# Kernel optimization log

Measured on AMD Instinct MI355X. Metric: run time of the kernel, lower is better.

The kernel has to match this reference:

```python
import jax, jax.numpy as jnp
import numpy as np

N = 100000        # nodes
E = 1600000       # edges (avg degree 16)
F_IN = 64         # num_node_features
NHID = 64         # args.nhid
NCLS = 16         # num_classes
K1 = 8            # Chebyshev order of conv1


def setup_inputs() -> dict:
    key = jax.random.key(0)
    k0, k1, k2, k3 = jax.random.split(key, 4)
    x = jax.random.normal(k0, (N, F_IN), dtype=jnp.float32)
    edge_index = jax.random.randint(k1, (2, E), 0, N, dtype=jnp.int32)
    # ChebConv params: K linear maps (no per-lin bias) + one shared bias
    W1 = jax.random.normal(k2, (K1, F_IN, NHID), dtype=jnp.float32) * (1.0 / np.sqrt(F_IN))
    b1 = jnp.zeros((NHID,), dtype=jnp.float32)
    W2 = jax.random.normal(k3, (1, NHID, NCLS), dtype=jnp.float32) * (1.0 / np.sqrt(NHID))
    b2 = jnp.zeros((NCLS,), dtype=jnp.float32)
    return {"x": x, "edge_index": edge_index, "W1": W1, "b1": b1, "W2": W2, "b2": b2}


def _cheb_norm(edge_index, num_nodes):
    # PyG ChebConv.__norm__ with normalization='sym', lambda_max=2.0, unit edge weights:
    # remove self loops; L_hat = 2L/lambda_max - I = -D^{-1/2} A D^{-1/2}, diag = 0.
    row, col = edge_index[0], edge_index[1]
    nonself = (row != col).astype(jnp.float32)
    deg = jax.ops.segment_sum(nonself, row, num_segments=num_nodes)
    dinv = jnp.where(deg > 0, jax.lax.rsqrt(jnp.maximum(deg, 1.0)), 0.0)
    norm = -dinv[row] * dinv[col] * nonself
    return row, col, norm


def reference(x, edge_index, W1, b1, W2, b2):
    row, col, norm = _cheb_norm(edge_index, N)

    def prop(h):  # L_hat @ h via gather + scatter-add, [N,F]
        return jax.ops.segment_sum(h[col] * norm[:, None], row, num_segments=N)

    # conv1: ChebConv K=8 recursion  Tx_k = 2*L_hat*Tx_{k-1} - Tx_{k-2}
    tx_prev = x
    out = x @ W1[0]
    tx = prop(x)
    out = out + tx @ W1[1]
    for k in range(2, K1):
        tx_new = 2.0 * prop(tx) - tx_prev
        out = out + tx_new @ W1[k]
        tx_prev, tx = tx, tx_new
    h = jax.nn.relu(out + b1)
    # dropout: identity (eval mode)
    # conv2: ChebConv K=1 -> just Tx_0 = h
    logits = h @ W2[0] + b2
    return jax.nn.softmax(logits, axis=1)
```

## Files before the change

### kernel.cpp

```cpp
#include <hip/hip_runtime.h>
#include <hip/hip_fp16.h>

#define N_NODES 100000
#define N_EDGES 1600000
#define F 64
#define NCLS 16
#define K1 8
#define BSH 9
#define NBK 196
#define BROWS 512
#define BKCAP 9216
#define EPB 4096

using f16x8 = __attribute__((ext_vector_type(8))) _Float16;
using f32x4 = __attribute__((ext_vector_type(4))) float;

__global__ __launch_bounds__(256) void k_bucketA(const int* __restrict__ ei,
                                                 int* __restrict__ gcur,
                                                 int2* __restrict__ bk) {
    __shared__ int cnt[4][256];
    __shared__ int wbase[4][256];
    int tid = threadIdx.x;
    int w = tid >> 6;
    for (int i = tid; i < 1024; i += 256) ((int*)cnt)[i] = 0;
    __syncthreads();
    int rv[16], cv[16], packed[16];
    int e0 = blockIdx.x * EPB;
#pragma unroll
    for (int u = 0; u < 16; u++) {
        int e = e0 + u * 256 + tid;
        packed[u] = -1;
        if (e < N_EDGES) {
            rv[u] = ei[e];
            cv[u] = ei[N_EDGES + e];
            if (rv[u] != cv[u]) {
                int b = rv[u] >> BSH;
                int rank = atomicAdd(&cnt[w][b], 1);
                packed[u] = (rank << 8) | b;
            }
        }
    }
    __syncthreads();
    {
        int c0 = cnt[0][tid], c1 = cnt[1][tid], c2 = cnt[2][tid], c3 = cnt[3][tid];
        int tot = c0 + c1 + c2 + c3;
        int g = tot ? atomicAdd(&gcur[tid], tot) : 0;
        wbase[0][tid] = g;
        wbase[1][tid] = g + c0;
        wbase[2][tid] = g + c0 + c1;
        wbase[3][tid] = g + c0 + c1 + c2;
    }
    __syncthreads();
#pragma unroll
    for (int u = 0; u < 16; u++) {
        if (packed[u] >= 0) {
            int b = packed[u] & 255;
            int rank = packed[u] >> 8;
            bk[(size_t)b * BKCAP + wbase[w][b] + rank] = make_int2(rv[u], cv[u]);
        }
    }
}

__global__ __launch_bounds__(256) void k_degB(const int2* __restrict__ bk,
                                              const int* __restrict__ gcur,
                                              int* __restrict__ deg,
                                              float* __restrict__ dinv,
                                              int* __restrict__ rowptr) {
    __shared__ int hist[BROWS];
    __shared__ int sd[256];
    int b = blockIdx.x;
    int tid = threadIdx.x;
    for (int i = tid; i < BROWS; i += 256) hist[i] = 0;
    __syncthreads();
    int cnt = gcur[b];
    const int2* src = bk + (size_t)b * BKCAP;
    for (int i = tid; i < cnt; i += 256)
        atomicAdd(&hist[src[i].x & (BROWS - 1)], 1);
    __syncthreads();
    int v0 = hist[2 * tid], v1 = hist[2 * tid + 1];
    int s = v0 + v1;
    sd[tid] = s;
    __syncthreads();
    for (int d = 1; d < 256; d <<= 1) {
        int t = (tid >= d) ? sd[tid - d] : 0;
        __syncthreads();
        sd[tid] += t;
        __syncthreads();
    }
    int excl = sd[tid] - s;
    int rbase = b << BSH;
    int cbase = b * BKCAP;
    int gr0 = rbase + 2 * tid;
    int gr1 = gr0 + 1;
    if (gr0 < N_NODES) {
        deg[gr0] = v0;
        dinv[gr0] = v0 > 0 ? rsqrtf((float)v0) : 0.f;
        rowptr[gr0] = cbase + excl;
    }
    if (gr1 < N_NODES) {
        deg[gr1] = v1;
        dinv[gr1] = v1 > 0 ? rsqrtf((float)v1) : 0.f;
        rowptr[gr1] = cbase + excl + v0;
    }
}

__global__ __launch_bounds__(256) void k_fillB(const int2* __restrict__ bk,
                                               const int* __restrict__ gcur,
                                               const int* __restrict__ rowptr,
                                               const float* __restrict__ dinv,
                                               int2* __restrict__ csr_ew) {
    __shared__ int cur[BROWS];
    int b = blockIdx.x;
    for (int i = threadIdx.x; i < BROWS; i += 256) cur[i] = 0;
    __syncthreads();
    int cnt = gcur[b];
    const int2* src = bk + (size_t)b * BKCAP;
    for (int i = threadIdx.x; i < cnt; i += 256) {
        int2 rc = src[i];
        int rank = atomicAdd(&cur[rc.x & (BROWS - 1)], 1);
        float w = -dinv[rc.x] * dinv[rc.y];
        csr_ew[rowptr[rc.x] + rank] = make_int2(rc.y, __float_as_int(w));
    }
}

__global__ void k_cvt(const float* __restrict__ x, __half* __restrict__ t0) {
    int i = blockIdx.x * blockDim.x + threadIdx.x;
    int base = i * 4;
    if (base >= N_NODES * F) return;
    float4 v = *(const float4*)&x[base];
    __half2 a = __floats2half2_rn(v.x, v.y);
    __half2 b = __floats2half2_rn(v.z, v.w);
    *(__half2*)&t0[base] = a;
    *(__half2*)&t0[base + 2] = b;
}

__global__ void k_prepW(const float* __restrict__ W1, __half* __restrict__ Wf) {
    int t = blockIdx.x * blockDim.x + threadIdx.x;
    if (t >= K1 * 2 * 4 * 64) return;
    int lane = t & 63;
    int cb = (t >> 6) & 3;
    int fg = (t >> 8) & 1;
    int kidx = t >> 9;
    int col = cb * 16 + (lane & 15);
    int kbase = fg * 32 + (lane >> 4) * 8;
    f16x8 v;
#pragma unroll
    for (int j = 0; j < 8; j++)
        v[j] = (_Float16)W1[kidx * 4096 + (kbase + j) * 64 + col];
    *(f16x8*)(Wf + (size_t)t * 8) = v;
}

__global__ __launch_bounds__(256) void k_prop(const int* __restrict__ rowptr,
                                              const int* __restrict__ deg,
                                              const int2* __restrict__ csr_ew,
                                              const __half* __restrict__ src,
                                              const __half* __restrict__ prev,
                                              __half* __restrict__ dst,
                                              float alpha, float beta) {
    int wpair = (int)((blockIdx.x * blockDim.x + threadIdx.x) >> 6);
    int lane = threadIdx.x & 63;
    int nA = wpair * 2;
    if (nA >= N_NODES) return;
    int h = lane >> 5;
    int hl = lane & 31;
    int s3 = (lane >> 3) & 3;
    int fb = (lane & 7) * 8;
    int node = nA + h;
    bool valid = node < N_NODES;
    int cb  = valid ? rowptr[node] : 0;
    int end = valid ? cb + deg[node] : 0;

    float acc[8] = {};

    while (true) {
        int n_own = end - cb;
        if (n_own > 32) n_own = 32;
        if (n_own < 0) n_own = 0;
        int n_oth = __shfl(n_own, lane ^ 32, 64);
        int nmax = n_own > n_oth ? n_own : n_oth;
        if (nmax == 0) break;
        int2 e = make_int2(0, 0);
        if (hl < n_own) e = csr_ew[cb + hl];
        for (int j = 0; j < nmax; j += 16) {
            int cc[4];
            float ww[4];
#pragma unroll
            for (int g = 0; g < 4; g++) {
                int sl = (h << 5) | (j + g * 4 + s3);
                cc[g] = __shfl(e.x, sl, 64);
                ww[g] = __int_as_float(__shfl(e.y, sl, 64));
            }
            uint4 raw[4];
#pragma unroll
            for (int g = 0; g < 4; g++)
                raw[g] = *(const uint4*)(src + (size_t)cc[g] * F + fb);
#pragma unroll
            for (int g = 0; g < 4; g++) {
                float2 f0 = __half22float2(*(__half2*)&raw[g].x);
                float2 f1 = __half22float2(*(__half2*)&raw[g].y);
                float2 f2 = __half22float2(*(__half2*)&raw[g].z);
                float2 f3 = __half22float2(*(__half2*)&raw[g].w);
                acc[0] = fmaf(ww[g], f0.x, acc[0]);
                acc[1] = fmaf(ww[g], f0.y, acc[1]);
                acc[2] = fmaf(ww[g], f1.x, acc[2]);
                acc[3] = fmaf(ww[g], f1.y, acc[3]);
                acc[4] = fmaf(ww[g], f2.x, acc[4]);
                acc[5] = fmaf(ww[g], f2.y, acc[5]);
                acc[6] = fmaf(ww[g], f3.x, acc[6]);
                acc[7] = fmaf(ww[g], f3.y, acc[7]);
            }
        }
        cb += n_own;
    }

#pragma unroll
    for (int i = 0; i < 8; i++) {
        acc[i] += __shfl_xor(acc[i], 8, 64);
        acc[i] += __shfl_xor(acc[i], 16, 64);
    }

    if ((lane & 24) == 0 && valid) {
        float r[8];
#pragma unroll
        for (int i = 0; i < 8; i++) r[i] = alpha * acc[i];
        if (beta != 0.f) {
            uint4 pv = *(const uint4*)(prev + (size_t)node * F + fb);
            float2 p0 = __half22float2(*(__half2*)&pv.x);
            float2 p1 = __half22float2(*(__half2*)&pv.y);
            float2 p2 = __half22float2(*(__half2*)&pv.z);
            float2 p3 = __half22float2(*(__half2*)&pv.w);
            r[0] -= beta * p0.x; r[1] -= beta * p0.y;
            r[2] -= beta * p1.x; r[3] -= beta * p1.y;
            r[4] -= beta * p2.x; r[5] -= beta * p2.y;
            r[6] -= beta * p3.x; r[7] -= beta * p3.y;
        }
        uint4 outv;
        *(__half2*)&outv.x = __floats2half2_rn(r[0], r[1]);
        *(__half2*)&outv.y = __floats2half2_rn(r[2], r[3]);
        *(__half2*)&outv.z = __floats2half2_rn(r[4], r[5]);
        *(__half2*)&outv.w = __floats2half2_rn(r[6], r[7]);
        *(uint4*)(dst + (size_t)node * F + fb) = outv;
    }
}

__global__ __launch_bounds__(256) void k_fused_mfma(const __half* __restrict__ T,
                                                    const __half* __restrict__ Wf,
                                                    const float* __restrict__ b1,
                                                    const float* __restrict__ W2,
                                                    const float* __restrict__ b2,
                                                    float* __restrict__ y) {
    __shared__ float Ht[64][65];
    __shared__ float W2l[64 * 16];
    __shared__ float b2l[16];
    int tid = threadIdx.x;
    int lane = tid & 63;
    int w = tid >> 6;
    int ln15 = lane & 15;
    int lg = lane >> 4;
    int base = blockIdx.x * 64;

    for (int j = tid; j < 64 * 16; j += 256) W2l[j] = W2[j];
    if (tid < 16) b2l[tid] = b2[tid];

    int nd = base + (w << 4) + ln15;
    if (nd > N_NODES - 1) nd = N_NODES - 1;

    f32x4 acc0 = {0.f, 0.f, 0.f, 0.f};
    f32x4 acc1 = {0.f, 0.f, 0.f, 0.f};
    f32x4 acc2 = {0.f, 0.f, 0.f, 0.f};
    f32x4 acc3 = {0.f, 0.f, 0.f, 0.f};

    for (int s = 0; s < 16; s++) {
        int kidx = s >> 1;
        int fg = s & 1;
        f16x8 a = *(const f16x8*)(T + ((size_t)kidx * N_NODES + nd) * F + fg * 32 + lg * 8);
        const __half* wb = Wf + ((size_t)((kidx * 2 + fg) * 4) * 64 + lane) * 8;
        f16x8 b0 = *(const f16x8*)(wb);
        f16x8 b1f = *(const f16x8*)(wb + 64 * 8);
        f16x8 b2f = *(const f16x8*)(wb + 128 * 8);
        f16x8 b3f = *(const f16x8*)(wb + 192 * 8);
        acc0 = __builtin_amdgcn_mfma_f32_16x16x32_f16(a, b0, acc0, 0, 0, 0);
        acc1 = __builtin_amdgcn_mfma_f32_16x16x32_f16(a, b1f, acc1, 0, 0, 0);
        acc2 = __builtin_amdgcn_mfma_f32_16x16x32_f16(a, b2f, acc2, 0, 0, 0);
        acc3 = __builtin_amdgcn_mfma_f32_16x16x32_f16(a, b3f, acc3, 0, 0, 0);
    }

    int hrow = (w << 4) + (lg << 2);
    {
        float bb0 = b1[0 * 16 + ln15];
        float bb1 = b1[1 * 16 + ln15];
        float bb2 = b1[2 * 16 + ln15];
        float bb3 = b1[3 * 16 + ln15];
#pragma unroll
        for (int r = 0; r < 4; r++) {
            float h0 = acc0[r] + bb0;
            float h1 = acc1[r] + bb1;
            float h2 = acc2[r] + bb2;
            float h3 = acc3[r] + bb3;
            Ht[hrow + r][0 * 16 + ln15] = h0 > 0.f ? h0 : 0.f;
            Ht[hrow + r][1 * 16 + ln15] = h1 > 0.f ? h1 : 0.f;
            Ht[hrow + r][2 * 16 + ln15] = h2 > 0.f ? h2 : 0.f;
            Ht[hrow + r][3 * 16 + ln15] = h3 > 0.f ? h3 : 0.f;
        }
    }
    __syncthreads();

    int node = tid >> 2;
    int cg = tid & 3;
    int gnode = base + node;
    if (gnode >= N_NODES) return;
    float l0 = b2l[cg * 4 + 0], l1 = b2l[cg * 4 + 1], l2 = b2l[cg * 4 + 2], l3 = b2l[cg * 4 + 3];
    for (int f = 0; f < 64; f++) {
        float h = Ht[node][f];
        l0 = fmaf(h, W2l[f * 16 + cg * 4 + 0], l0);
        l1 = fmaf(h, W2l[f * 16 + cg * 4 + 1], l1);
        l2 = fmaf(h, W2l[f * 16 + cg * 4 + 2], l2);
        l3 = fmaf(h, W2l[f * 16 + cg * 4 + 3], l3);
    }
    float m = fmaxf(fmaxf(l0, l1), fmaxf(l2, l3));
    m = fmaxf(m, __shfl_xor(m, 1, 64));
    m = fmaxf(m, __shfl_xor(m, 2, 64));
    float e0 = expf(l0 - m), e1 = expf(l1 - m), e2 = expf(l2 - m), e3 = expf(l3 - m);
    float s = e0 + e1 + e2 + e3;
    s += __shfl_xor(s, 1, 64);
    s += __shfl_xor(s, 2, 64);
    float inv = 1.f / s;
    float4 o = make_float4(e0 * inv, e1 * inv, e2 * inv, e3 * inv);
    *(float4*)&y[(size_t)gnode * 16 + cg * 4] = o;
}


extern "C" void kernel_launch(void* const* d_in, const int* in_sizes, int n_in,
                              void* d_out, int out_size, void* d_ws, size_t ws_size,
                              hipStream_t stream) {
    const float* x  = (const float*)d_in[0];
    const int*   ei = (const int*)d_in[1];
    const float* W1 = (const float*)d_in[2];
    const float* b1 = (const float*)d_in[3];
    const float* W2 = (const float*)d_in[4];
    const float* b2 = (const float*)d_in[5];
    float* y = (float*)d_out;

    char* p = (char*)d_ws;
    auto alloc = [&](size_t bytes) {
        char* q = p;
        p += (bytes + 255) & ~(size_t)255;
        return q;
    };
    int*   deg    = (int*)alloc((size_t)N_NODES * 4);
    float* dinv   = (float*)alloc((size_t)N_NODES * 4);
    int*   rowptr = (int*)alloc((size_t)(N_NODES + 1) * 4);
    int*   gcur   = (int*)alloc(256 * 4);
    int2*  csr_ew = (int2*)alloc((size_t)NBK * BKCAP * 8);
    __half* T     = (__half*)alloc((size_t)K1 * N_NODES * F * 2);
    __half* Wf    = (__half*)alloc((size_t)K1 * 2 * 4 * 64 * 8 * 2);

    int2* bk = (int2*)T;

    hipMemsetAsync(gcur, 0, 256 * 4, stream);

    k_bucketA<<<(N_EDGES + EPB - 1) / EPB, 256, 0, stream>>>(ei, gcur, bk);
    k_degB<<<NBK, 256, 0, stream>>>(bk, gcur, deg, dinv, rowptr);
    k_fillB<<<NBK, 256, 0, stream>>>(bk, gcur, rowptr, dinv, csr_ew);
    k_prepW<<<16, 256, 0, stream>>>(W1, Wf);

    const size_t TSZ = (size_t)N_NODES * F;
    __half* Tk[K1];
    for (int k = 0; k < K1; k++) Tk[k] = T + (size_t)k * TSZ;

    k_cvt<<<(N_NODES * F / 4 + 255) / 256, 256, 0, stream>>>(x, Tk[0]);

    int npair = (N_NODES + 1) / 2;
    int prop_blocks = (npair + 3) / 4;
    k_prop<<<prop_blocks, 256, 0, stream>>>(rowptr, deg, csr_ew, Tk[0], Tk[0], Tk[1], 1.f, 0.f);
    for (int k = 2; k < K1; k++)
        k_prop<<<prop_blocks, 256, 0, stream>>>(rowptr, deg, csr_ew, Tk[k - 1], Tk[k - 2], Tk[k], 2.f, 1.f);

    int gemm_blocks = (N_NODES + 63) / 64;
    k_fused_mfma<<<gemm_blocks, 256, 0, stream>>>(T, Wf, b1, W2, b2, y);
}
```

Measured before the change: 324.6 us.

## Pack bucketed edges into 32 bits, fuse CSR fill into degree kernel, recompute edge weights

Bucketed edges are packed as a single 32-bit word holding the local row and the column, which halves bucket traffic. The degree/rowptr kernel now also does the per-bucket counting sort in shared memory and writes a column-only CSR, which removes the separate fill kernel. The propagation kernel stores only column indices and computes the weight as dinv[col] per edge, with -dinv[row] applied once per node. This halves CSR bytes read per edge but adds a dependent gather of dinv for each edge. The 36 KB shared-memory sort buffer may also lower occupancy of the CSR kernel.

```diff
diff --git a/kernel.cpp b/kernel.cpp
--- a/kernel.cpp
+++ b/kernel.cpp
@@ -11,30 +11,32 @@
 #define BROWS 512
 #define BKCAP 9216
 #define EPB 4096
+#define COLBITS 17
 
 using f16x8 = __attribute__((ext_vector_type(8))) _Float16;
 using f32x4 = __attribute__((ext_vector_type(4))) float;
 
 __global__ __launch_bounds__(256) void k_bucketA(const int* __restrict__ ei,
                                                  int* __restrict__ gcur,
-                                                 int2* __restrict__ bk) {
+                                                 unsigned* __restrict__ bk) {
     __shared__ int cnt[4][256];
     __shared__ int wbase[4][256];
     int tid = threadIdx.x;
     int w = tid >> 6;
     for (int i = tid; i < 1024; i += 256) ((int*)cnt)[i] = 0;
     __syncthreads();
-    int rv[16], cv[16], packed[16];
+    unsigned pe[16];
+    int packed[16];
     int e0 = blockIdx.x * EPB;
 #pragma unroll
     for (int u = 0; u < 16; u++) {
         int e = e0 + u * 256 + tid;
         packed[u] = -1;
         if (e < N_EDGES) {
-            rv[u] = ei[e];
-            cv[u] = ei[N_EDGES + e];
-            if (rv[u] != cv[u]) {
-                int b = rv[u] >> BSH;
+            int r = ei[e], c = ei[N_EDGES + e];
+            if (r != c) {
+                int b = r >> BSH;
+                pe[u] = ((unsigned)(r & (BROWS - 1)) << COLBITS) | (unsigned)c;
                 int rank = atomicAdd(&cnt[w][b], 1);
                 packed[u] = (rank << 8) | b;
             }
@@ -56,26 +58,29 @@
         if (packed[u] >= 0) {
             int b = packed[u] & 255;
             int rank = packed[u] >> 8;
-            bk[(size_t)b * BKCAP + wbase[w][b] + rank] = make_int2(rv[u], cv[u]);
-        }
-    }
-}
-
-__global__ __launch_bounds__(256) void k_degB(const int2* __restrict__ bk,
+            bk[(size_t)b * BKCAP + wbase[w][b] + rank] = pe[u];
+        }
+    }
+}
+
+__global__ __launch_bounds__(256) void k_csrB(const unsigned* __restrict__ bk,
                                               const int* __restrict__ gcur,
                                               int* __restrict__ deg,
                                               float* __restrict__ dinv,
-                                              int* __restrict__ rowptr) {
+                                              int* __restrict__ rowptr,
+                                              int* __restrict__ csr_col) {
     __shared__ int hist[BROWS];
+    __shared__ int cur[BROWS];
     __shared__ int sd[256];
+    __shared__ int sorted[BKCAP];
     int b = blockIdx.x;
     int tid = threadIdx.x;
-    for (int i = tid; i < BROWS; i += 256) hist[i] = 0;
+    for (int i = tid; i < BROWS; i += 256) { hist[i] = 0; cur[i] = 0; }
     __syncthreads();
     int cnt = gcur[b];
-    const int2* src = bk + (size_t)b * BKCAP;
+    const unsigned* src = bk + (size_t)b * BKCAP;
     for (int i = tid; i < cnt; i += 256)
-        atomicAdd(&hist[src[i].x & (BROWS - 1)], 1);
+        atomicAdd(&hist[src[i] >> COLBITS], 1);
     __syncthreads();
     int v0 = hist[2 * tid], v1 = hist[2 * tid + 1];
     int s = v0 + v1;
@@ -102,25 +107,19 @@
         dinv[gr1] = v1 > 0 ? rsqrtf((float)v1) : 0.f;
         rowptr[gr1] = cbase + excl + v0;
     }
-}
-
-__global__ __launch_bounds__(256) void k_fillB(const int2* __restrict__ bk,
-                                               const int* __restrict__ gcur,
-                                               const int* __restrict__ rowptr,
-                                               const float* __restrict__ dinv,
-                                               int2* __restrict__ csr_ew) {
-    __shared__ int cur[BROWS];
-    int b = blockIdx.x;
-    for (int i = threadIdx.x; i < BROWS; i += 256) cur[i] = 0;
-    __syncthreads();
-    int cnt = gcur[b];
-    const int2* src = bk + (size_t)b * BKCAP;
-    for (int i = threadIdx.x; i < cnt; i += 256) {
-        int2 rc = src[i];
-        int rank = atomicAdd(&cur[rc.x & (BROWS - 1)], 1);
-        float w = -dinv[rc.x] * dinv[rc.y];
-        csr_ew[rowptr[rc.x] + rank] = make_int2(rc.y, __float_as_int(w));
-    }
+    __syncthreads();
+    hist[2 * tid] = excl;
+    hist[2 * tid + 1] = excl + v0;
+    __syncthreads();
+    for (int i = tid; i < cnt; i += 256) {
+        unsigned e = src[i];
+        int rl = e >> COLBITS;
+        int pos = hist[rl] + atomicAdd(&cur[rl], 1);
+        sorted[pos] = (int)(e & ((1u << COLBITS) - 1));
+    }
+    __syncthreads();
+    for (int i = tid; i < cnt; i += 256)
+        csr_col[cbase + i] = sorted[i];
 }
 
 __global__ void k_cvt(const float* __restrict__ x, __half* __restrict__ t0) {
@@ -152,7 +151,8 @@
 
 __global__ __launch_bounds__(256) void k_prop(const int* __restrict__ rowptr,
                                               const int* __restrict__ deg,
-                                              const int2* __restrict__ csr_ew,
+                                              const int* __restrict__ csr_col,
+                                              const float* __restrict__ dinv,
                                               const __half* __restrict__ src,
                                               const __half* __restrict__ prev,
                                               __half* __restrict__ dst,
@@ -169,6 +169,7 @@
     bool valid = node < N_NODES;
     int cb  = valid ? rowptr[node] : 0;
     int end = valid ? cb + deg[node] : 0;
+    float dn = valid ? dinv[node] : 0.f;
 
     float acc[8] = {};
 
@@ -179,16 +180,20 @@
         int n_oth = __shfl(n_own, lane ^ 32, 64);
         int nmax = n_own > n_oth ? n_own : n_oth;
         if (nmax == 0) break;
-        int2 e = make_int2(0, 0);
-        if (hl < n_own) e = csr_ew[cb + hl];
+        int col = 0;
+        float dv = 0.f;
+        if (hl < n_own) {
+            col = csr_col[cb + hl];
+            dv = dinv[col];
+        }
         for (int j = 0; j < nmax; j += 16) {
             int cc[4];
             float ww[4];
 #pragma unroll
             for (int g = 0; g < 4; g++) {
                 int sl = (h << 5) | (j + g * 4 + s3);
-                cc[g] = __shfl(e.x, sl, 64);
-                ww[g] = __int_as_float(__shfl(e.y, sl, 64));
+                cc[g] = __shfl(col, sl, 64);
+                ww[g] = __shfl(dv, sl, 64);
             }
             uint4 raw[4];
 #pragma unroll
@@ -220,9 +225,10 @@
     }
 
     if ((lane & 24) == 0 && valid) {
+        float scale = -alpha * dn;
         float r[8];
 #pragma unroll
-        for (int i = 0; i < 8; i++) r[i] = alpha * acc[i];
+        for (int i = 0; i < 8; i++) r[i] = scale * acc[i];
         if (beta != 0.f) {
             uint4 pv = *(const uint4*)(prev + (size_t)node * F + fb);
             float2 p0 = __half22float2(*(__half2*)&pv.x);
@@ -347,21 +353,20 @@
         p += (bytes + 255) & ~(size_t)255;
         return q;
     };
-    int*   deg    = (int*)alloc((size_t)N_NODES * 4);
-    float* dinv   = (float*)alloc((size_t)N_NODES * 4);
-    int*   rowptr = (int*)alloc((size_t)(N_NODES + 1) * 4);
-    int*   gcur   = (int*)alloc(256 * 4);
-    int2*  csr_ew = (int2*)alloc((size_t)NBK * BKCAP * 8);
-    __half* T     = (__half*)alloc((size_t)K1 * N_NODES * F * 2);
-    __half* Wf    = (__half*)alloc((size_t)K1 * 2 * 4 * 64 * 8 * 2);
-
-    int2* bk = (int2*)T;
+    int*   deg     = (int*)alloc((size_t)N_NODES * 4);
+    float* dinv    = (float*)alloc((size_t)N_NODES * 4);
+    int*   rowptr  = (int*)alloc((size_t)N_NODES * 4);
+    int*   gcur    = (int*)alloc(256 * 4);
+    int*   csr_col = (int*)alloc((size_t)NBK * BKCAP * 4);
+    __half* T      = (__half*)alloc((size_t)K1 * N_NODES * F * 2);
+    __half* Wf     = (__half*)alloc((size_t)K1 * 2 * 4 * 64 * 8 * 2);
+
+    unsigned* bk = (unsigned*)T;
 
     hipMemsetAsync(gcur, 0, 256 * 4, stream);
 
     k_bucketA<<<(N_EDGES + EPB - 1) / EPB, 256, 0, stream>>>(ei, gcur, bk);
-    k_degB<<<NBK, 256, 0, stream>>>(bk, gcur, deg, dinv, rowptr);
-    k_fillB<<<NBK, 256, 0, stream>>>(bk, gcur, rowptr, dinv, csr_ew);
+    k_csrB<<<NBK, 256, 0, stream>>>(bk, gcur, deg, dinv, rowptr, csr_col);
     k_prepW<<<16, 256, 0, stream>>>(W1, Wf);
 
     const size_t TSZ = (size_t)N_NODES * F;
@@ -372,9 +377,9 @@
 
     int npair = (N_NODES + 1) / 2;
     int prop_blocks = (npair + 3) / 4;
-    k_prop<<<prop_blocks, 256, 0, stream>>>(rowptr, deg, csr_ew, Tk[0], Tk[0], Tk[1], 1.f, 0.f);
+    k_prop<<<prop_blocks, 256, 0, stream>>>(rowptr, deg, csr_col, dinv, Tk[0], Tk[0], Tk[1], 1.f, 0.f);
     for (int k = 2; k < K1; k++)
-        k_prop<<<prop_blocks, 256, 0, stream>>>(rowptr, deg, csr_ew, Tk[k - 1], Tk[k - 2], Tk[k], 2.f, 1.f);
+        k_prop<<<prop_blocks, 256, 0, stream>>>(rowptr, deg, csr_col, dinv, Tk[k - 1], Tk[k - 2], Tk[k], 2.f, 1.f);
 
     int gemm_blocks = (N_NODES + 63) / 64;
     k_fused_mfma<<<gemm_blocks, 256, 0, stream>>>(T, Wf, b1, W2, b2, y);
```

Result: faster. 307.8 us (-5.2%).
